# Kernel tuning notes

Measured on AMD Instinct MI355X. Metric: run time of the kernel, lower is better.

The kernel has to match this reference:

```python
import jax, jax.numpy as jnp
import numpy as np

N_NODES = 20000
N_EDGES = 200000
N_FEAT = 2048   # number_of_labels
H1 = 512        # GATE_hidden_size_1
H2 = 30         # GATE_hidden_size_2


def setup_inputs() -> dict:
    key = jax.random.key(0)
    ks = jax.random.split(key, 6)
    s = 0.05
    features = jax.random.normal(ks[0], (N_NODES, N_FEAT), dtype=jnp.float32)
    edge_index = jax.random.randint(ks[1], (2, N_EDGES), 0, N_NODES)
    W1 = jax.random.normal(ks[2], (N_FEAT, H1), dtype=jnp.float32) * s
    att_src1 = jax.random.normal(ks[3], (H1,), dtype=jnp.float32) * s
    att_dst1 = jax.random.normal(ks[4], (H1,), dtype=jnp.float32) * s
    W2 = jax.random.normal(ks[5], (H1, H2), dtype=jnp.float32) * s
    return {"features": features, "edge_index": edge_index,
            "W1": W1, "att_src1": att_src1, "att_dst1": att_dst1, "W2": W2}


def _segment_softmax(e, seg, n):
    # softmax over edges grouped by destination node (every node has a self loop)
    m = jax.ops.segment_max(e, seg, num_segments=n)
    ex = jnp.exp(e - m[seg])
    den = jax.ops.segment_sum(ex, seg, num_segments=n)
    return ex / den[seg]


def _gat_propagate(xw, a_src, a_dst, src, dst, n):
    # STAGATE GATConv message: alpha = sigmoid(a_src[j] + a_dst[i]), segment-softmax, scatter-add
    e = jax.nn.sigmoid(a_src[src] + a_dst[dst])          # [E]
    coef = _segment_softmax(e, dst, n)                   # [E]
    msg = xw[src] * coef[:, None]                        # [E, C] gather + scale
    return jax.ops.segment_sum(msg, dst, num_segments=n)  # [N, C] scatter-add


def reference(features, edge_index, W1, att_src1, att_dst1, W2):
    n = features.shape[0]
    loops = jnp.arange(n, dtype=edge_index.dtype)
    src = jnp.concatenate([edge_index[0], loops])  # add_self_loops=True
    dst = jnp.concatenate([edge_index[1], loops])

    # conv1 (attention=True): computes and stores node-level attention logits
    xw1 = features @ W1                 # [N, H1]
    a1s = xw1 @ att_src1                # [N]
    a1d = xw1 @ att_dst1                # [N]
    h1 = jax.nn.elu(_gat_propagate(xw1, a1s, a1d, src, dst, n))

    # conv2 (attention=False): plain linear transform, no propagation
    h2 = h1 @ W2                        # [N, H2]
    norm = jnp.sqrt(jnp.sum(h2 * h2, axis=1, keepdims=True))
    h2 = h2 / jnp.maximum(norm, 1e-12)  # F.normalize(dim=1)

    # conv3: weight tied to W2^T, attention tied to conv1's logits
    xw3 = h2 @ W2.T                     # [N, H1]
    h3 = jax.nn.elu(_gat_propagate(xw3, a1s, a1d, src, dst, n))

    # conv4 (attention=False): weight tied to W1^T
    h4 = h3 @ W1.T                      # [N, N_FEAT]

    return jnp.mean((features - h4) ** 2)  # F.mse_loss
```

## Files before the change

kernel.cpp:

```cpp
#include <hip/hip_runtime.h>
#include <math.h>

#define N_NODES 20000
#define N_EDGESI 200000
#define E_TOT   220000
#define N_FEAT  2048
#define H1      512
#define H2      30

typedef __bf16 bf16x8 __attribute__((ext_vector_type(8)));
typedef float  floatx4 __attribute__((ext_vector_type(4)));

__device__ __forceinline__ unsigned short f2bf(float f) {
    unsigned int u = __float_as_uint(f);
    unsigned int r = (u + 0x7FFF + ((u >> 16) & 1)) >> 16;
    return (unsigned short)r;
}
__device__ __forceinline__ float bf2f(unsigned short u) {
    return __uint_as_float(((unsigned int)u) << 16);
}
__device__ __forceinline__ unsigned int packtrunc(float a, float b) {
    return (__float_as_uint(a) >> 16) | (__float_as_uint(b) & 0xFFFF0000u);
}
__device__ __forceinline__ unsigned int packrne(float a, float b) {
    return (unsigned int)f2bf(a) | ((unsigned int)f2bf(b) << 16);
}

__global__ __launch_bounds__(256) void cvtW1(const float* __restrict__ W1,
                                             unsigned short* __restrict__ w1bf,
                                             unsigned short* __restrict__ w1tbf) {
    __shared__ float tile[32][33];
    const int bk = blockIdx.y * 32, bn = blockIdx.x * 32;
    const int tc = threadIdx.x & 31, tr = threadIdx.x >> 5;
    for (int r = tr; r < 32; r += 8) {
        float v = W1[(size_t)(bk + r) * H1 + bn + tc];
        w1bf[(size_t)(bk + r) * H1 + bn + tc] = f2bf(v);
        tile[r][tc] = v;
    }
    __syncthreads();
    for (int r = tr; r < 32; r += 8) {
        w1tbf[(size_t)(bn + r) * N_FEAT + bk + tc] = f2bf(tile[tc][r]);
    }
}

__global__ __launch_bounds__(256, 5) void gemm1_mfma(const float* __restrict__ A,
                                                     const unsigned short* __restrict__ Bt,
                                                     unsigned short* __restrict__ C,
                                                     const float* __restrict__ atts,
                                                     const float* __restrict__ attd,
                                                     float* __restrict__ a1s,
                                                     float* __restrict__ a1d) {
    __shared__ unsigned short As[2][64 * 40];
    __shared__ unsigned short Bs[2][128 * 40];
    const int blk = blockIdx.x;
    const int xcd = blk & 7, rr = blk >> 3;
    const int ntile = rr & 3, group = rr >> 2;
    const int stripe = group * 8 + xcd;
    if (stripe >= 313) return;
    const int bm = stripe * 64, bn = ntile * 128;
    const int t = threadIdx.x;
    const int lane = t & 63, w = t >> 6;
    const int wm = w >> 1, wn = w & 1;
    const int ln = lane & 15, qd = lane >> 4;
    const int r0 = t >> 2, cs = (t & 3) * 8;

    int gra = bm + r0;        if (gra > N_NODES - 1) gra = N_NODES - 1;
    const float* ap0 = A + (size_t)gra * N_FEAT + cs;
    const unsigned short* bp0 = Bt + (size_t)(bn + r0) * N_FEAT + cs;
    const unsigned short* bp1 = Bt + (size_t)(bn + r0 + 64) * N_FEAT + cs;

    floatx4 acc[2][4];
#pragma unroll
    for (int i = 0; i < 2; i++)
#pragma unroll
        for (int j = 0; j < 4; j++) acc[i][j] = (floatx4){0.f, 0.f, 0.f, 0.f};

    float4 pa00 = *(const float4*)(ap0);
    float4 pa01 = *(const float4*)(ap0 + 4);
    uint4  pb0  = *(const uint4*)(bp0);
    uint4  pb1  = *(const uint4*)(bp1);
    {
        uint4 pk0;
        pk0.x = packtrunc(pa00.x, pa00.y); pk0.y = packtrunc(pa00.z, pa00.w);
        pk0.z = packtrunc(pa01.x, pa01.y); pk0.w = packtrunc(pa01.z, pa01.w);
        *(uint4*)&As[0][r0 * 40 + cs] = pk0;
        *(uint4*)&Bs[0][r0 * 40 + cs] = pb0;
        *(uint4*)&Bs[0][(r0 + 64) * 40 + cs] = pb1;
    }
    pa00 = *(const float4*)(ap0 + 32);
    pa01 = *(const float4*)(ap0 + 36);
    pb0  = *(const uint4*)(bp0 + 32);
    pb1  = *(const uint4*)(bp1 + 32);
    __syncthreads();

    int cur = 0;
    for (int k0 = 0; k0 < N_FEAT; k0 += 32) {
        bf16x8 af[2], bfr[4];
        const unsigned short* Ab = &As[cur][(wm * 32 + ln) * 40 + qd * 8];
        const unsigned short* Bb = &Bs[cur][(wn * 64 + ln) * 40 + qd * 8];
#pragma unroll
        for (int i = 0; i < 2; i++) af[i]  = *(const bf16x8*)(const void*)(Ab + i * 16 * 40);
#pragma unroll
        for (int j = 0; j < 4; j++) bfr[j] = *(const bf16x8*)(const void*)(Bb + j * 16 * 40);
        if (k0 + 32 < N_FEAT) {
            uint4 pk0;
            pk0.x = packtrunc(pa00.x, pa00.y); pk0.y = packtrunc(pa00.z, pa00.w);
            pk0.z = packtrunc(pa01.x, pa01.y); pk0.w = packtrunc(pa01.z, pa01.w);
            const int nb = cur ^ 1;
            *(uint4*)&As[nb][r0 * 40 + cs] = pk0;
            *(uint4*)&Bs[nb][r0 * 40 + cs] = pb0;
            *(uint4*)&Bs[nb][(r0 + 64) * 40 + cs] = pb1;
            if (k0 + 64 < N_FEAT) {
                const int kn = k0 + 64;
                pa00 = *(const float4*)(ap0 + kn);
                pa01 = *(const float4*)(ap0 + kn + 4);
                pb0  = *(const uint4*)(bp0 + kn);
                pb1  = *(const uint4*)(bp1 + kn);
            }
        }
#pragma unroll
        for (int i = 0; i < 2; i++)
#pragma unroll
            for (int j = 0; j < 4; j++)
                acc[i][j] = __builtin_amdgcn_mfma_f32_16x16x32_bf16(af[i], bfr[j], acc[i][j], 0, 0, 0);
        if (k0 + 32 < N_FEAT) __syncthreads();
        cur ^= 1;
    }

#pragma unroll
    for (int i = 0; i < 2; i++)
#pragma unroll
        for (int j = 0; j < 4; j++)
#pragma unroll
            for (int p = 0; p < 4; p++) {
                int m = bm + wm * 32 + i * 16 + qd * 4 + p;
                if (m < N_NODES) {
                    int n = bn + wn * 64 + j * 16 + ln;
                    C[(size_t)m * H1 + n] = f2bf(acc[i][j][p]);
                }
            }
    float avs[4], avd[4];
#pragma unroll
    for (int j = 0; j < 4; j++) {
        int n = bn + wn * 64 + j * 16 + ln;
        avs[j] = atts[n];
        avd[j] = attd[n];
    }
#pragma unroll
    for (int i = 0; i < 2; i++)
#pragma unroll
        for (int p = 0; p < 4; p++) {
            float vs = 0.f, vd = 0.f;
#pragma unroll
            for (int j = 0; j < 4; j++) {
                vs += acc[i][j][p] * avs[j];
                vd += acc[i][j][p] * avd[j];
            }
#pragma unroll
            for (int msk = 1; msk < 16; msk <<= 1) {
                vs += __shfl_xor(vs, msk);
                vd += __shfl_xor(vd, msk);
            }
            if (ln == p) {
                int m = bm + wm * 32 + i * 16 + qd * 4 + p;
                if (m < N_NODES) {
                    unsafeAtomicAdd(a1s + m, vs);
                    unsafeAtomicAdd(a1d + m, vd);
                }
            }
        }
}

__global__ __launch_bounds__(256) void gemm4_mse(const unsigned short* __restrict__ A,
                                                 const unsigned short* __restrict__ B,
                                                 const float* __restrict__ F,
                                                 float* __restrict__ partial) {
    __shared__ unsigned short As[128 * 40];
    __shared__ unsigned short Bs[128 * 40];
    __shared__ float red[256];
    const int blk = blockIdx.x;
    const int xcd = blk & 7, rr = blk >> 3;
    const int ntile = rr & 15, group = rr >> 4;
    const int stripe = group * 8 + xcd;
    if (stripe >= 157) return;
    const int bm = stripe * 128, bn = ntile * 128;
    const int t = threadIdx.x;
    const int lane = t & 63, w = t >> 6;
    const int wm = w >> 1, wn = w & 1;
    const int ln = lane & 15, qd = lane >> 4;
    const int r0 = t >> 2, cs = (t & 3) * 8;

    int gr0 = bm + r0;        if (gr0 > N_NODES - 1) gr0 = N_NODES - 1;
    int gr1 = bm + r0 + 64;   if (gr1 > N_NODES - 1) gr1 = N_NODES - 1;
    const unsigned short* ap0 = A + (size_t)gr0 * H1 + cs;
    const unsigned short* ap1 = A + (size_t)gr1 * H1 + cs;
    const unsigned short* bp0 = B + (size_t)(bn + r0) * H1 + cs;
    const unsigned short* bp1 = B + (size_t)(bn + r0 + 64) * H1 + cs;

    floatx4 acc[4][4];
#pragma unroll
    for (int i = 0; i < 4; i++)
#pragma unroll
        for (int j = 0; j < 4; j++) acc[i][j] = (floatx4){0.f, 0.f, 0.f, 0.f};

    uint4 pa0 = *(const uint4*)(ap0);
    uint4 pa1 = *(const uint4*)(ap1);
    uint4 pb0 = *(const uint4*)(bp0);
    uint4 pb1 = *(const uint4*)(bp1);

    for (int k0 = 0; k0 < H1; k0 += 32) {
        *(uint4*)&As[r0 * 40 + cs] = pa0;
        *(uint4*)&As[(r0 + 64) * 40 + cs] = pa1;
        *(uint4*)&Bs[r0 * 40 + cs] = pb0;
        *(uint4*)&Bs[(r0 + 64) * 40 + cs] = pb1;
        __syncthreads();
        const bool more = (k0 + 32) < H1;
        if (more) {
            int kn = k0 + 32;
            pa0 = *(const uint4*)(ap0 + kn);
            pa1 = *(const uint4*)(ap1 + kn);
            pb0 = *(const uint4*)(bp0 + kn);
            pb1 = *(const uint4*)(bp1 + kn);
        }
        bf16x8 af[4], bfr[4];
        const unsigned short* Ab = As + (size_t)(wm * 64 + ln) * 40 + qd * 8;
        const unsigned short* Bb = Bs + (size_t)(wn * 64 + ln) * 40 + qd * 8;
#pragma unroll
        for (int i = 0; i < 4; i++) af[i]  = *(const bf16x8*)(const void*)(Ab + i * 16 * 40);
#pragma unroll
        for (int j = 0; j < 4; j++) bfr[j] = *(const bf16x8*)(const void*)(Bb + j * 16 * 40);
#pragma unroll
        for (int i = 0; i < 4; i++)
#pragma unroll
            for (int j = 0; j < 4; j++)
                acc[i][j] = __builtin_amdgcn_mfma_f32_16x16x32_bf16(af[i], bfr[j], acc[i][j], 0, 0, 0);
        __syncthreads();
    }
    float sum = 0.f;
#pragma unroll
    for (int i = 0; i < 4; i++)
#pragma unroll
        for (int j = 0; j < 4; j++)
#pragma unroll
            for (int p = 0; p < 4; p++) {
                int m = bm + wm * 64 + i * 16 + qd * 4 + p;
                if (m < N_NODES) {
                    int n = bn + wn * 64 + j * 16 + ln;
                    float fv = F[(size_t)m * N_FEAT + n];
                    float d = fv - acc[i][j][p];
                    sum += d * d;
                }
            }
    red[t] = sum;
    __syncthreads();
    for (int off = 128; off; off >>= 1) {
        if (t < off) red[t] += red[t + off];
        __syncthreads();
    }
    if (t == 0) unsafeAtomicAdd(partial, red[0]);
}

__global__ void edge_att(const int* __restrict__ ei,
                         const float* __restrict__ a1s,
                         const float* __restrict__ a1d,
                         float* __restrict__ ebuf,
                         float* __restrict__ den,
                         int* __restrict__ deg) {
    int e = blockIdx.x * blockDim.x + threadIdx.x;
    if (e >= E_TOT) return;
    int s, d;
    if (e < N_EDGESI) { s = ei[e]; d = ei[N_EDGESI + e]; }
    else { s = e - N_EDGESI; d = s; }
    float x = a1s[s] + a1d[d];
    float sig = 1.f / (1.f + __expf(-x));
    float ex = __expf(sig);
    ebuf[e] = ex;
    unsafeAtomicAdd(&den[d], ex);
    atomicAdd(&deg[d], 1);
}

__global__ __launch_bounds__(1024) void scan_k(const int* __restrict__ deg,
                                               int* __restrict__ off) {
    __shared__ int wsum[16];
    __shared__ int carry_s;
    const int lane = threadIdx.x & 63, wid = threadIdx.x >> 6;
    if (threadIdx.x == 0) carry_s = 0;
    __syncthreads();
    for (int base = 0; base < N_NODES; base += 1024) {
        int i = base + threadIdx.x;
        int v = (i < N_NODES) ? deg[i] : 0;
        int x = v;
#pragma unroll
        for (int s = 1; s < 64; s <<= 1) {
            int tt = __shfl_up(x, s);
            if (lane >= s) x += tt;
        }
        if (lane == 63) wsum[wid] = x;
        __syncthreads();
        if (wid == 0 && lane < 16) {
            int wv = wsum[lane];
#pragma unroll
            for (int s = 1; s < 16; s <<= 1) {
                int tt = __shfl_up(wv, s);
                if (lane >= s) wv += tt;
            }
            wsum[lane] = wv;
        }
        __syncthreads();
        int wbase = (wid == 0) ? 0 : wsum[wid - 1];
        int c = carry_s;
        int incl = x + wbase + c;
        if (i < N_NODES) off[i] = incl - v;
        __syncthreads();
        if (threadIdx.x == 0) carry_s = c + wsum[15];
        __syncthreads();
    }
}

__global__ void bucket_k(const int* __restrict__ ei,
                         const float* __restrict__ ebuf,
                         const float* __restrict__ den,
                         int* __restrict__ cursor,
                         int* __restrict__ csr_src,
                         float* __restrict__ csr_coef) {
    int e = blockIdx.x * blockDim.x + threadIdx.x;
    if (e >= E_TOT) return;
    int s, d;
    if (e < N_EDGESI) { s = ei[e]; d = ei[N_EDGESI + e]; }
    else { s = e - N_EDGESI; d = s; }
    int pos = atomicAdd(&cursor[d], 1);
    csr_src[pos] = s;
    csr_coef[pos] = ebuf[e] / den[d];
}

__global__ __launch_bounds__(256) void gather_elu_bf(const int* __restrict__ off,
                                                     const int* __restrict__ csr_src,
                                                     const float* __restrict__ csr_coef,
                                                     const unsigned short* __restrict__ X,
                                                     unsigned short* __restrict__ Y) {
    int d = blockIdx.x * 4 + (threadIdx.x >> 6);
    int lane = threadIdx.x & 63;
    if (d >= N_NODES) return;
    int beg = off[d];
    int end = (d == N_NODES - 1) ? E_TOT : off[d + 1];
    float a[8] = {0.f, 0.f, 0.f, 0.f, 0.f, 0.f, 0.f, 0.f};
    float b[8] = {0.f, 0.f, 0.f, 0.f, 0.f, 0.f, 0.f, 0.f};
    int j = beg;
    for (; j + 1 < end; j += 2) {
        int s0 = csr_src[j], s1 = csr_src[j + 1];
        float c0 = csr_coef[j], c1 = csr_coef[j + 1];
        uint4 raw0 = *(const uint4*)(X + (size_t)s0 * H1 + lane * 8);
        uint4 raw1 = *(const uint4*)(X + (size_t)s1 * H1 + lane * 8);
        a[0] += __uint_as_float(raw0.x << 16) * c0;
        a[1] += __uint_as_float(raw0.x & 0xFFFF0000u) * c0;
        a[2] += __uint_as_float(raw0.y << 16) * c0;
        a[3] += __uint_as_float(raw0.y & 0xFFFF0000u) * c0;
        a[4] += __uint_as_float(raw0.z << 16) * c0;
        a[5] += __uint_as_float(raw0.z & 0xFFFF0000u) * c0;
        a[6] += __uint_as_float(raw0.w << 16) * c0;
        a[7] += __uint_as_float(raw0.w & 0xFFFF0000u) * c0;
        b[0] += __uint_as_float(raw1.x << 16) * c1;
        b[1] += __uint_as_float(raw1.x & 0xFFFF0000u) * c1;
        b[2] += __uint_as_float(raw1.y << 16) * c1;
        b[3] += __uint_as_float(raw1.y & 0xFFFF0000u) * c1;
        b[4] += __uint_as_float(raw1.z << 16) * c1;
        b[5] += __uint_as_float(raw1.z & 0xFFFF0000u) * c1;
        b[6] += __uint_as_float(raw1.w << 16) * c1;
        b[7] += __uint_as_float(raw1.w & 0xFFFF0000u) * c1;
    }
    if (j < end) {
        int s0 = csr_src[j];
        float c0 = csr_coef[j];
        uint4 raw0 = *(const uint4*)(X + (size_t)s0 * H1 + lane * 8);
        a[0] += __uint_as_float(raw0.x << 16) * c0;
        a[1] += __uint_as_float(raw0.x & 0xFFFF0000u) * c0;
        a[2] += __uint_as_float(raw0.y << 16) * c0;
        a[3] += __uint_as_float(raw0.y & 0xFFFF0000u) * c0;
        a[4] += __uint_as_float(raw0.z << 16) * c0;
        a[5] += __uint_as_float(raw0.z & 0xFFFF0000u) * c0;
        a[6] += __uint_as_float(raw0.w << 16) * c0;
        a[7] += __uint_as_float(raw0.w & 0xFFFF0000u) * c0;
    }
#pragma unroll
    for (int e = 0; e < 8; e++) {
        float v = a[e] + b[e];
        a[e] = v > 0.f ? v : __expf(v) - 1.f;
    }
    uint4 o;
    o.x = packrne(a[0], a[1]);
    o.y = packrne(a[2], a[3]);
    o.z = packrne(a[4], a[5]);
    o.w = packrne(a[6], a[7]);
    *(uint4*)(Y + (size_t)d * H1 + lane * 8) = o;
}

__global__ __launch_bounds__(256) void gemm2_norm_bf(const unsigned short* __restrict__ H1b,
                                                     const float* __restrict__ W2,
                                                     float* __restrict__ h2n) {
    __shared__ float hs[8 * 516];
    const int n0 = blockIdx.x * 8;
    const int tid = threadIdx.x;
    for (int idx = tid; idx < 512; idx += 256) {
        int r = idx >> 6, c = (idx & 63) * 8;
        uint4 raw = *(const uint4*)(H1b + (size_t)(n0 + r) * H1 + c);
        float* hp = hs + r * 516 + c;
        hp[0] = __uint_as_float(raw.x << 16);
        hp[1] = __uint_as_float(raw.x & 0xFFFF0000u);
        hp[2] = __uint_as_float(raw.y << 16);
        hp[3] = __uint_as_float(raw.y & 0xFFFF0000u);
        hp[4] = __uint_as_float(raw.z << 16);
        hp[5] = __uint_as_float(raw.z & 0xFFFF0000u);
        hp[6] = __uint_as_float(raw.w << 16);
        hp[7] = __uint_as_float(raw.w & 0xFFFF0000u);
    }
    __syncthreads();
    const int sub = tid >> 5, j = tid & 31;
    float a0 = 0.f, a1 = 0.f, a2 = 0.f, a3 = 0.f;
    if (j < H2) {
        const float* hr = hs + sub * 516;
        for (int k = 0; k < H1; k += 4) {
            a0 += hr[k] * W2[k * H2 + j];
            a1 += hr[k + 1] * W2[(k + 1) * H2 + j];
            a2 += hr[k + 2] * W2[(k + 2) * H2 + j];
            a3 += hr[k + 3] * W2[(k + 3) * H2 + j];
        }
    }
    float acc = (a0 + a1) + (a2 + a3);
    float sq = acc * acc;
    for (int m = 16; m; m >>= 1) sq += __shfl_xor(sq, m, 32);
    float inv = 1.f / fmaxf(sqrtf(sq), 1e-12f);
    if (j < H2) h2n[(size_t)(n0 + sub) * H2 + j] = acc * inv;
}

#define G3_CHUNK 40
__global__ __launch_bounds__(256) void gemm3_k(const float* __restrict__ h2n,
                                               const float* __restrict__ W2,
                                               unsigned short* __restrict__ xw3) {
    const int t = threadIdx.x;
    const int h0 = t << 1;
    float w0[H2], w1[H2];
#pragma unroll
    for (int k = 0; k < H2; k++) {
        w0[k] = W2[(size_t)h0 * H2 + k];
        w1[k] = W2[(size_t)h0 * H2 + H2 + k];
    }
    const int n0 = blockIdx.x * G3_CHUNK;
    const int nend = (n0 + G3_CHUNK < N_NODES) ? n0 + G3_CHUNK : N_NODES;
    for (int n = n0; n < nend; n++) {
        const float* hr = h2n + (size_t)n * H2;
        float a0 = 0.f, a1 = 0.f;
#pragma unroll
        for (int k = 0; k < H2; k++) {
            float hv = hr[k];
            a0 += hv * w0[k];
            a1 += hv * w1[k];
        }
        *(unsigned int*)(xw3 + (size_t)n * H1 + h0) = packrne(a0, a1);
    }
}

__global__ void finalize_k(const float* __restrict__ partial, float* __restrict__ out) {
    out[0] = partial[0] * (1.f / ((float)N_NODES * (float)N_FEAT));
}

extern "C" void kernel_launch(void* const* d_in, const int* in_sizes, int n_in,
                              void* d_out, int out_size, void* d_ws, size_t ws_size,
                              hipStream_t stream) {
    const float* features = (const float*)d_in[0];
    const int*   ei       = (const int*)d_in[1];
    const float* W1       = (const float*)d_in[2];
    const float* atts     = (const float*)d_in[3];
    const float* attd     = (const float*)d_in[4];
    const float* W2       = (const float*)d_in[5];
    float* out = (float*)d_out;

    char* ws = (char*)d_ws;
    unsigned short* xw1bf = (unsigned short*)(ws);
    unsigned short* h3bf  = (unsigned short*)(ws + 20480000);
    unsigned short* h1bf  = (unsigned short*)(ws + 40960000);
    unsigned short* w1bf  = (unsigned short*)(ws + 61440000);
    unsigned short* w1tbf = (unsigned short*)(ws + 63537152);
    float* h2n      = (float*)(ws + 65634304);
    float* a1s      = (float*)(ws + 68034304);
    float* a1d      = (float*)(ws + 68114304);
    float* den      = (float*)(ws + 68194304);
    int*   deg      = (int*)  (ws + 68274304);
    float* partial  = (float*)(ws + 68354304);
    float* ebuf     = (float*)(ws + 68354320);
    int*   off      = (int*)  (ws + 69234320);
    int*   cursor   = (int*)  (ws + 69314320);
    int*   csr_src  = (int*)  (ws + 69394320);
    float* csr_coef = (float*)(ws + 70274320);

    hipMemsetAsync(a1s, 0, 320016, stream);

    cvtW1<<<dim3(16, 64), 256, 0, stream>>>(W1, w1bf, w1tbf);

    gemm1_mfma<<<1280, 256, 0, stream>>>(features, w1tbf, xw1bf, atts, attd, a1s, a1d);

    edge_att<<<(E_TOT + 255) / 256, 256, 0, stream>>>(ei, a1s, a1d, ebuf, den, deg);

    scan_k<<<1, 1024, 0, stream>>>(deg, off);
    hipMemcpyAsync(cursor, off, 20000 * 4, hipMemcpyDeviceToDevice, stream);
    bucket_k<<<(E_TOT + 255) / 256, 256, 0, stream>>>(ei, ebuf, den, cursor, csr_src, csr_coef);

    gather_elu_bf<<<N_NODES / 4, 256, 0, stream>>>(off, csr_src, csr_coef, xw1bf, h1bf);

    gemm2_norm_bf<<<N_NODES / 8, 256, 0, stream>>>(h1bf, W2, h2n);

    gemm3_k<<<(N_NODES + G3_CHUNK - 1) / G3_CHUNK, 256, 0, stream>>>(h2n, W2, xw1bf);

    gather_elu_bf<<<N_NODES / 4, 256, 0, stream>>>(off, csr_src, csr_coef, xw1bf, h3bf);

    gemm4_mse<<<2560, 256, 0, stream>>>(h3bf, w1bf, features, partial);

    finalize_k<<<1, 1, 0, stream>>>(partial, out);
}
```

Before: 626.5 us.

## Use direct global-to-LDS loads with triple-buffered swizzled pipeline in GEMMs

Both the first GEMM and the final GEMM+MSE kernel now stage tiles via global_load_lds (direct global-to-LDS DMA) into three rotating XOR-swizzled LDS buffers, with waitcnt-based barriers that keep two stages in flight. In gemm1 the fp32 feature tile is now stored as fp32 in LDS and truncated to bf16 at fragment load time rather than before the LDS store. The aim is to remove register round-trips and hide global latency better, at the cost of more LDS per block (occupancy hints lowered to 3) and doubled LDS traffic for the fp32 A tile.

```diff
diff --git a/kernel.cpp b/kernel.cpp
--- a/kernel.cpp
+++ b/kernel.cpp
@@ -11,19 +11,33 @@
 typedef __bf16 bf16x8 __attribute__((ext_vector_type(8)));
 typedef float  floatx4 __attribute__((ext_vector_type(4)));
 
+__device__ __forceinline__ void gl16(const void* g, void* l) {
+    __builtin_amdgcn_global_load_lds(
+        (const __attribute__((address_space(1))) unsigned int*)g,
+        (__attribute__((address_space(3))) unsigned int*)l, 16, 0, 0);
+}
+__device__ __forceinline__ void stage_barrier4() {
+    asm volatile("s_waitcnt vmcnt(4) lgkmcnt(0)" ::: "memory");
+    __builtin_amdgcn_s_barrier();
+}
+__device__ __forceinline__ void stage_barrier0() {
+    asm volatile("s_waitcnt vmcnt(0) lgkmcnt(0)" ::: "memory");
+    __builtin_amdgcn_s_barrier();
+}
+
 __device__ __forceinline__ unsigned short f2bf(float f) {
     unsigned int u = __float_as_uint(f);
     unsigned int r = (u + 0x7FFF + ((u >> 16) & 1)) >> 16;
     return (unsigned short)r;
 }
-__device__ __forceinline__ float bf2f(unsigned short u) {
-    return __uint_as_float(((unsigned int)u) << 16);
-}
 __device__ __forceinline__ unsigned int packtrunc(float a, float b) {
     return (__float_as_uint(a) >> 16) | (__float_as_uint(b) & 0xFFFF0000u);
 }
 __device__ __forceinline__ unsigned int packrne(float a, float b) {
     return (unsigned int)f2bf(a) | ((unsigned int)f2bf(b) << 16);
+}
+__device__ __forceinline__ bf16x8 u4_to_bf(uint4 u) {
+    union { uint4 u; bf16x8 b; } cv; cv.u = u; return cv.b;
 }
 
 __global__ __launch_bounds__(256) void cvtW1(const float* __restrict__ W1,
@@ -43,15 +57,15 @@
     }
 }
 
-__global__ __launch_bounds__(256, 5) void gemm1_mfma(const float* __restrict__ A,
+__global__ __launch_bounds__(256, 3) void gemm1_mfma(const float* __restrict__ A,
                                                      const unsigned short* __restrict__ Bt,
                                                      unsigned short* __restrict__ C,
                                                      const float* __restrict__ atts,
                                                      const float* __restrict__ attd,
                                                      float* __restrict__ a1s,
                                                      float* __restrict__ a1d) {
-    __shared__ unsigned short As[2][64 * 40];
-    __shared__ unsigned short Bs[2][128 * 40];
+    __shared__ float          Asb[3][64 * 32];
+    __shared__ unsigned short Bsb[3][128 * 32];
     const int blk = blockIdx.x;
     const int xcd = blk & 7, rr = blk >> 3;
     const int ntile = rr & 3, group = rr >> 2;
@@ -62,12 +76,41 @@
     const int lane = t & 63, w = t >> 6;
     const int wm = w >> 1, wn = w & 1;
     const int ln = lane & 15, qd = lane >> 4;
-    const int r0 = t >> 2, cs = (t & 3) * 8;
-
-    int gra = bm + r0;        if (gra > N_NODES - 1) gra = N_NODES - 1;
-    const float* ap0 = A + (size_t)gra * N_FEAT + cs;
-    const unsigned short* bp0 = Bt + (size_t)(bn + r0) * N_FEAT + cs;
-    const unsigned short* bp1 = Bt + (size_t)(bn + r0 + 64) * N_FEAT + cs;
+
+    const int ci0 = t, ci1 = t + 256;
+    const int ar0 = ci0 >> 3, ap0 = ci0 & 7;
+    const int ar1 = ci1 >> 3, ap1 = ci1 & 7;
+    int gra0 = bm + ar0; if (gra0 > N_NODES - 1) gra0 = N_NODES - 1;
+    int gra1 = bm + ar1; if (gra1 > N_NODES - 1) gra1 = N_NODES - 1;
+    const float* gA0 = A + (size_t)gra0 * N_FEAT + ((ap0 ^ (ar0 & 7)) << 2);
+    const float* gA1 = A + (size_t)gra1 * N_FEAT + ((ap1 ^ (ar1 & 7)) << 2);
+    const int ldsA0 = ci0 * 4, ldsA1 = ci1 * 4;
+    const int br0 = ci0 >> 2, bp0 = ci0 & 3;
+    const int br1 = ci1 >> 2, bp1 = ci1 & 3;
+    const unsigned short* gB0 = Bt + (size_t)(bn + br0) * N_FEAT + ((bp0 ^ ((br0 >> 1) & 3)) << 3);
+    const unsigned short* gB1 = Bt + (size_t)(bn + br1) * N_FEAT + ((bp1 ^ ((br1 >> 1) & 3)) << 3);
+    const int ldsB0 = ci0 * 8, ldsB1 = ci1 * 8;
+
+#define STAGE1(k0, Ab, Bb) do { \
+        gl16(gA0 + (k0), (Ab) + ldsA0); \
+        gl16(gA1 + (k0), (Ab) + ldsA1); \
+        gl16(gB0 + (k0), (Bb) + ldsB0); \
+        gl16(gB1 + (k0), (Bb) + ldsB1); \
+    } while (0)
+
+    int offA[2][2], offB[4];
+#pragma unroll
+    for (int i = 0; i < 2; i++) {
+        int row = wm * 32 + i * 16 + ln;
+#pragma unroll
+        for (int h = 0; h < 2; h++)
+            offA[i][h] = row * 32 + (((qd * 2 + h) ^ (row & 7)) << 2);
+    }
+#pragma unroll
+    for (int j = 0; j < 4; j++) {
+        int row = wn * 64 + j * 16 + ln;
+        offB[j] = row * 32 + ((qd ^ ((row >> 1) & 3)) << 3);
+    }
 
     floatx4 acc[2][4];
 #pragma unroll
@@ -75,57 +118,42 @@
 #pragma unroll
         for (int j = 0; j < 4; j++) acc[i][j] = (floatx4){0.f, 0.f, 0.f, 0.f};
 
-    float4 pa00 = *(const float4*)(ap0);
-    float4 pa01 = *(const float4*)(ap0 + 4);
-    uint4  pb0  = *(const uint4*)(bp0);
-    uint4  pb1  = *(const uint4*)(bp1);
-    {
-        uint4 pk0;
-        pk0.x = packtrunc(pa00.x, pa00.y); pk0.y = packtrunc(pa00.z, pa00.w);
-        pk0.z = packtrunc(pa01.x, pa01.y); pk0.w = packtrunc(pa01.z, pa01.w);
-        *(uint4*)&As[0][r0 * 40 + cs] = pk0;
-        *(uint4*)&Bs[0][r0 * 40 + cs] = pb0;
-        *(uint4*)&Bs[0][(r0 + 64) * 40 + cs] = pb1;
-    }
-    pa00 = *(const float4*)(ap0 + 32);
-    pa01 = *(const float4*)(ap0 + 36);
-    pb0  = *(const uint4*)(bp0 + 32);
-    pb1  = *(const uint4*)(bp1 + 32);
-    __syncthreads();
-
-    int cur = 0;
-    for (int k0 = 0; k0 < N_FEAT; k0 += 32) {
-        bf16x8 af[2], bfr[4];
-        const unsigned short* Ab = &As[cur][(wm * 32 + ln) * 40 + qd * 8];
-        const unsigned short* Bb = &Bs[cur][(wn * 64 + ln) * 40 + qd * 8];
-#pragma unroll
-        for (int i = 0; i < 2; i++) af[i]  = *(const bf16x8*)(const void*)(Ab + i * 16 * 40);
-#pragma unroll
-        for (int j = 0; j < 4; j++) bfr[j] = *(const bf16x8*)(const void*)(Bb + j * 16 * 40);
-        if (k0 + 32 < N_FEAT) {
-            uint4 pk0;
-            pk0.x = packtrunc(pa00.x, pa00.y); pk0.y = packtrunc(pa00.z, pa00.w);
-            pk0.z = packtrunc(pa01.x, pa01.y); pk0.w = packtrunc(pa01.z, pa01.w);
-            const int nb = cur ^ 1;
-            *(uint4*)&As[nb][r0 * 40 + cs] = pk0;
-            *(uint4*)&Bs[nb][r0 * 40 + cs] = pb0;
-            *(uint4*)&Bs[nb][(r0 + 64) * 40 + cs] = pb1;
-            if (k0 + 64 < N_FEAT) {
-                const int kn = k0 + 64;
-                pa00 = *(const float4*)(ap0 + kn);
-                pa01 = *(const float4*)(ap0 + kn + 4);
-                pb0  = *(const uint4*)(bp0 + kn);
-                pb1  = *(const uint4*)(bp1 + kn);
-            }
-        }
-#pragma unroll
-        for (int i = 0; i < 2; i++)
-#pragma unroll
-            for (int j = 0; j < 4; j++)
-                acc[i][j] = __builtin_amdgcn_mfma_f32_16x16x32_bf16(af[i], bfr[j], acc[i][j], 0, 0, 0);
-        if (k0 + 32 < N_FEAT) __syncthreads();
-        cur ^= 1;
-    }
+#define COMPUTE1(Ab, Bb) do { \
+        bf16x8 af_[2], bf_[4]; \
+        _Pragma("unroll") for (int j = 0; j < 4; j++) \
+            bf_[j] = *(const bf16x8*)(const void*)((Bb) + offB[j]); \
+        _Pragma("unroll") for (int i = 0; i < 2; i++) { \
+            float4 f0 = *(const float4*)((Ab) + offA[i][0]); \
+            float4 f1 = *(const float4*)((Ab) + offA[i][1]); \
+            uint4 pk; \
+            pk.x = packtrunc(f0.x, f0.y); pk.y = packtrunc(f0.z, f0.w); \
+            pk.z = packtrunc(f1.x, f1.y); pk.w = packtrunc(f1.z, f1.w); \
+            af_[i] = u4_to_bf(pk); } \
+        _Pragma("unroll") for (int i = 0; i < 2; i++) \
+        _Pragma("unroll") for (int j = 0; j < 4; j++) \
+            acc[i][j] = __builtin_amdgcn_mfma_f32_16x16x32_bf16(af_[i], bf_[j], acc[i][j], 0, 0, 0); \
+    } while (0)
+
+    float *Ac = Asb[0], *An1 = Asb[1], *An2 = Asb[2];
+    unsigned short *Bc = Bsb[0], *Bn1 = Bsb[1], *Bn2 = Bsb[2];
+    STAGE1(0, Ac, Bc);
+    STAGE1(32, An1, Bn1);
+    stage_barrier4();
+
+    for (int k = 0; k < 62; ++k) {
+        STAGE1((k + 2) * 32, An2, Bn2);
+        COMPUTE1(Ac, Bc);
+        stage_barrier4();
+        float* ta = Ac; Ac = An1; An1 = An2; An2 = ta;
+        unsigned short* tb = Bc; Bc = Bn1; Bn1 = Bn2; Bn2 = tb;
+    }
+    COMPUTE1(Ac, Bc);
+    stage_barrier0();
+    { float* ta = Ac; Ac = An1; An1 = An2; An2 = ta;
+      unsigned short* tb = Bc; Bc = Bn1; Bn1 = Bn2; Bn2 = tb; }
+    COMPUTE1(Ac, Bc);
+#undef STAGE1
+#undef COMPUTE1
 
 #pragma unroll
     for (int i = 0; i < 2; i++)
@@ -171,12 +199,12 @@
         }
 }
 
-__global__ __launch_bounds__(256) void gemm4_mse(const unsigned short* __restrict__ A,
-                                                 const unsigned short* __restrict__ B,
-                                                 const float* __restrict__ F,
-                                                 float* __restrict__ partial) {
-    __shared__ unsigned short As[128 * 40];
-    __shared__ unsigned short Bs[128 * 40];
+__global__ __launch_bounds__(256, 3) void gemm4_mse(const unsigned short* __restrict__ Ah,
+                                                    const unsigned short* __restrict__ B,
+                                                    const float* __restrict__ F,
+                                                    float* __restrict__ partial) {
+    __shared__ unsigned short Asb[3][128 * 32];
+    __shared__ unsigned short Bsb[3][128 * 32];
     __shared__ float red[256];
     const int blk = blockIdx.x;
     const int xcd = blk & 7, rr = blk >> 3;
@@ -188,14 +216,36 @@
     const int lane = t & 63, w = t >> 6;
     const int wm = w >> 1, wn = w & 1;
     const int ln = lane & 15, qd = lane >> 4;
-    const int r0 = t >> 2, cs = (t & 3) * 8;
-
-    int gr0 = bm + r0;        if (gr0 > N_NODES - 1) gr0 = N_NODES - 1;
-    int gr1 = bm + r0 + 64;   if (gr1 > N_NODES - 1) gr1 = N_NODES - 1;
-    const unsigned short* ap0 = A + (size_t)gr0 * H1 + cs;
-    const unsigned short* ap1 = A + (size_t)gr1 * H1 + cs;
-    const unsigned short* bp0 = B + (size_t)(bn + r0) * H1 + cs;
-    const unsigned short* bp1 = B + (size_t)(bn + r0 + 64) * H1 + cs;
+
+    const int ci0 = t, ci1 = t + 256;
+    const int r0c = ci0 >> 2, p0c = ci0 & 3;
+    const int r1c = ci1 >> 2, p1c = ci1 & 3;
+    int gra0 = bm + r0c; if (gra0 > N_NODES - 1) gra0 = N_NODES - 1;
+    int gra1 = bm + r1c; if (gra1 > N_NODES - 1) gra1 = N_NODES - 1;
+    const unsigned short* gA0 = Ah + (size_t)gra0 * H1 + ((p0c ^ ((r0c >> 1) & 3)) << 3);
+    const unsigned short* gA1 = Ah + (size_t)gra1 * H1 + ((p1c ^ ((r1c >> 1) & 3)) << 3);
+    const unsigned short* gB0 = B + (size_t)(bn + r0c) * H1 + ((p0c ^ ((r0c >> 1) & 3)) << 3);
+    const unsigned short* gB1 = B + (size_t)(bn + r1c) * H1 + ((p1c ^ ((r1c >> 1) & 3)) << 3);
+    const int lds0 = ci0 * 8, lds1 = ci1 * 8;
+
+#define STAGE4(k0, Ab, Bb) do { \
+        gl16(gA0 + (k0), (Ab) + lds0); \
+        gl16(gA1 + (k0), (Ab) + lds1); \
+        gl16(gB0 + (k0), (Bb) + lds0); \
+        gl16(gB1 + (k0), (Bb) + lds1); \
+    } while (0)
+
+    int offA[4], offB[4];
+#pragma unroll
+    for (int i = 0; i < 4; i++) {
+        int row = wm * 64 + i * 16 + ln;
+        offA[i] = row * 32 + ((qd ^ ((row >> 1) & 3)) << 3);
+    }
+#pragma unroll
+    for (int j = 0; j < 4; j++) {
+        int row = wn * 64 + j * 16 + ln;
+        offB[j] = row * 32 + ((qd ^ ((row >> 1) & 3)) << 3);
+    }
 
     floatx4 acc[4][4];
 #pragma unroll
@@ -203,39 +253,38 @@
 #pragma unroll
         for (int j = 0; j < 4; j++) acc[i][j] = (floatx4){0.f, 0.f, 0.f, 0.f};
 
-    uint4 pa0 = *(const uint4*)(ap0);
-    uint4 pa1 = *(const uint4*)(ap1);
-    uint4 pb0 = *(const uint4*)(bp0);
-    uint4 pb1 = *(const uint4*)(bp1);
-
-    for (int k0 = 0; k0 < H1; k0 += 32) {
-        *(uint4*)&As[r0 * 40 + cs] = pa0;
-        *(uint4*)&As[(r0 + 64) * 40 + cs] = pa1;
-        *(uint4*)&Bs[r0 * 40 + cs] = pb0;
-        *(uint4*)&Bs[(r0 + 64) * 40 + cs] = pb1;
-        __syncthreads();
-        const bool more = (k0 + 32) < H1;
-        if (more) {
-            int kn = k0 + 32;
-            pa0 = *(const uint4*)(ap0 + kn);
-            pa1 = *(const uint4*)(ap1 + kn);
-            pb0 = *(const uint4*)(bp0 + kn);
-            pb1 = *(const uint4*)(bp1 + kn);
-        }
-        bf16x8 af[4], bfr[4];
-        const unsigned short* Ab = As + (size_t)(wm * 64 + ln) * 40 + qd * 8;
-        const unsigned short* Bb = Bs + (size_t)(wn * 64 + ln) * 40 + qd * 8;
-#pragma unroll
-        for (int i = 0; i < 4; i++) af[i]  = *(const bf16x8*)(const void*)(Ab + i * 16 * 40);
-#pragma unroll
-        for (int j = 0; j < 4; j++) bfr[j] = *(const bf16x8*)(const void*)(Bb + j * 16 * 40);
-#pragma unroll
-        for (int i = 0; i < 4; i++)
-#pragma unroll
-            for (int j = 0; j < 4; j++)
-                acc[i][j] = __builtin_amdgcn_mfma_f32_16x16x32_bf16(af[i], bfr[j], acc[i][j], 0, 0, 0);
-        __syncthreads();
-    }
+#define COMPUTE4(Ab, Bb) do { \
+        bf16x8 af_[4], bf_[4]; \
+        _Pragma("unroll") for (int i = 0; i < 4; i++) \
+            af_[i] = *(const bf16x8*)(const void*)((Ab) + offA[i]); \
+        _Pragma("unroll") for (int j = 0; j < 4; j++) \
+            bf_[j] = *(const bf16x8*)(const void*)((Bb) + offB[j]); \
+        _Pragma("unroll") for (int i = 0; i < 4; i++) \
+        _Pragma("unroll") for (int j = 0; j < 4; j++) \
+            acc[i][j] = __builtin_amdgcn_mfma_f32_16x16x32_bf16(af_[i], bf_[j], acc[i][j], 0, 0, 0); \
+    } while (0)
+
+    unsigned short *Ac = Asb[0], *An1 = Asb[1], *An2 = Asb[2];
+    unsigned short *Bc = Bsb[0], *Bn1 = Bsb[1], *Bn2 = Bsb[2];
+    STAGE4(0, Ac, Bc);
+    STAGE4(32, An1, Bn1);
+    stage_barrier4();
+
+    for (int k = 0; k < 14; ++k) {
+        STAGE4((k + 2) * 32, An2, Bn2);
+        COMPUTE4(Ac, Bc);
+        stage_barrier4();
+        unsigned short* ta = Ac; Ac = An1; An1 = An2; An2 = ta;
+        unsigned short* tb = Bc; Bc = Bn1; Bn1 = Bn2; Bn2 = tb;
+    }
+    COMPUTE4(Ac, Bc);
+    stage_barrier0();
+    { unsigned short* ta = Ac; Ac = An1; An1 = An2; An2 = ta;
+      unsigned short* tb = Bc; Bc = Bn1; Bn1 = Bn2; Bn2 = tb; }
+    COMPUTE4(Ac, Bc);
+#undef STAGE4
+#undef COMPUTE4
+
     float sum = 0.f;
 #pragma unroll
     for (int i = 0; i < 4; i++)
```

Result: slower. 651.5 us (+4.0%).

## Load B fragments directly to registers in GEMMs, shrink gemm4 tile

Applied to the files above, without the earlier changes.

Both MFMA GEMMs (gemm1 and gemm4) now skip staging the B operand through LDS. Each lane loads its B fragment straight from global memory into registers, double-buffered two k-steps ahead. Only A is staged in a double-buffered LDS tile, and the barrier becomes a manual lgkmcnt wait plus s_barrier. gemm4 moves to 64-row tiles with twice the blocks and a 5-wave occupancy hint, which cuts LDS traffic and barrier cost. In exchange, B reads are less coalesced per lane (16 rows × 16 bytes each), register pressure rises, and gemm4 reads B twice as often overall.

```diff
diff --git a/kernel.cpp b/kernel.cpp
--- a/kernel.cpp
+++ b/kernel.cpp
@@ -11,19 +11,24 @@
 typedef __bf16 bf16x8 __attribute__((ext_vector_type(8)));
 typedef float  floatx4 __attribute__((ext_vector_type(4)));
 
+__device__ __forceinline__ void lds_barrier() {
+    asm volatile("s_waitcnt lgkmcnt(0)" ::: "memory");
+    __builtin_amdgcn_s_barrier();
+}
+
 __device__ __forceinline__ unsigned short f2bf(float f) {
     unsigned int u = __float_as_uint(f);
     unsigned int r = (u + 0x7FFF + ((u >> 16) & 1)) >> 16;
     return (unsigned short)r;
 }
-__device__ __forceinline__ float bf2f(unsigned short u) {
-    return __uint_as_float(((unsigned int)u) << 16);
-}
 __device__ __forceinline__ unsigned int packtrunc(float a, float b) {
     return (__float_as_uint(a) >> 16) | (__float_as_uint(b) & 0xFFFF0000u);
 }
 __device__ __forceinline__ unsigned int packrne(float a, float b) {
     return (unsigned int)f2bf(a) | ((unsigned int)f2bf(b) << 16);
+}
+__device__ __forceinline__ bf16x8 u4_to_bf(uint4 u) {
+    union { uint4 u; bf16x8 b; } cv; cv.u = u; return cv.b;
 }
 
 __global__ __launch_bounds__(256) void cvtW1(const float* __restrict__ W1,
@@ -51,7 +56,6 @@
                                                      float* __restrict__ a1s,
                                                      float* __restrict__ a1d) {
     __shared__ unsigned short As[2][64 * 40];
-    __shared__ unsigned short Bs[2][128 * 40];
     const int blk = blockIdx.x;
     const int xcd = blk & 7, rr = blk >> 3;
     const int ntile = rr & 3, group = rr >> 2;
@@ -64,10 +68,16 @@
     const int ln = lane & 15, qd = lane >> 4;
     const int r0 = t >> 2, cs = (t & 3) * 8;
 
-    int gra = bm + r0;        if (gra > N_NODES - 1) gra = N_NODES - 1;
-    const float* ap0 = A + (size_t)gra * N_FEAT + cs;
-    const unsigned short* bp0 = Bt + (size_t)(bn + r0) * N_FEAT + cs;
-    const unsigned short* bp1 = Bt + (size_t)(bn + r0 + 64) * N_FEAT + cs;
+    int gra = bm + r0; if (gra > N_NODES - 1) gra = N_NODES - 1;
+    const float* apA = A + (size_t)gra * N_FEAT + cs;
+
+    const unsigned short* bfp[4];
+#pragma unroll
+    for (int j = 0; j < 4; j++)
+        bfp[j] = Bt + (size_t)(bn + wn * 64 + j * 16 + ln) * N_FEAT + qd * 8;
+
+    const int offA0 = (wm * 32 + ln) * 40 + qd * 8;
+    const int offA1 = (wm * 32 + 16 + ln) * 40 + qd * 8;
 
     floatx4 acc[2][4];
 #pragma unroll
@@ -75,57 +85,58 @@
 #pragma unroll
         for (int j = 0; j < 4; j++) acc[i][j] = (floatx4){0.f, 0.f, 0.f, 0.f};
 
-    float4 pa00 = *(const float4*)(ap0);
-    float4 pa01 = *(const float4*)(ap0 + 4);
-    uint4  pb0  = *(const uint4*)(bp0);
-    uint4  pb1  = *(const uint4*)(bp1);
     {
-        uint4 pk0;
-        pk0.x = packtrunc(pa00.x, pa00.y); pk0.y = packtrunc(pa00.z, pa00.w);
-        pk0.z = packtrunc(pa01.x, pa01.y); pk0.w = packtrunc(pa01.z, pa01.w);
-        *(uint4*)&As[0][r0 * 40 + cs] = pk0;
-        *(uint4*)&Bs[0][r0 * 40 + cs] = pb0;
-        *(uint4*)&Bs[0][(r0 + 64) * 40 + cs] = pb1;
-    }
-    pa00 = *(const float4*)(ap0 + 32);
-    pa01 = *(const float4*)(ap0 + 36);
-    pb0  = *(const uint4*)(bp0 + 32);
-    pb1  = *(const uint4*)(bp1 + 32);
-    __syncthreads();
-
-    int cur = 0;
-    for (int k0 = 0; k0 < N_FEAT; k0 += 32) {
-        bf16x8 af[2], bfr[4];
-        const unsigned short* Ab = &As[cur][(wm * 32 + ln) * 40 + qd * 8];
-        const unsigned short* Bb = &Bs[cur][(wn * 64 + ln) * 40 + qd * 8];
-#pragma unroll
-        for (int i = 0; i < 2; i++) af[i]  = *(const bf16x8*)(const void*)(Ab + i * 16 * 40);
-#pragma unroll
-        for (int j = 0; j < 4; j++) bfr[j] = *(const bf16x8*)(const void*)(Bb + j * 16 * 40);
-        if (k0 + 32 < N_FEAT) {
-            uint4 pk0;
-            pk0.x = packtrunc(pa00.x, pa00.y); pk0.y = packtrunc(pa00.z, pa00.w);
-            pk0.z = packtrunc(pa01.x, pa01.y); pk0.w = packtrunc(pa01.z, pa01.w);
-            const int nb = cur ^ 1;
-            *(uint4*)&As[nb][r0 * 40 + cs] = pk0;
-            *(uint4*)&Bs[nb][r0 * 40 + cs] = pb0;
-            *(uint4*)&Bs[nb][(r0 + 64) * 40 + cs] = pb1;
-            if (k0 + 64 < N_FEAT) {
-                const int kn = k0 + 64;
-                pa00 = *(const float4*)(ap0 + kn);
-                pa01 = *(const float4*)(ap0 + kn + 4);
-                pb0  = *(const uint4*)(bp0 + kn);
-                pb1  = *(const uint4*)(bp1 + kn);
-            }
-        }
-#pragma unroll
-        for (int i = 0; i < 2; i++)
-#pragma unroll
-            for (int j = 0; j < 4; j++)
-                acc[i][j] = __builtin_amdgcn_mfma_f32_16x16x32_bf16(af[i], bfr[j], acc[i][j], 0, 0, 0);
-        if (k0 + 32 < N_FEAT) __syncthreads();
-        cur ^= 1;
-    }
+        float4 a0 = *(const float4*)(apA);
+        float4 a1 = *(const float4*)(apA + 4);
+        uint4 pk;
+        pk.x = packtrunc(a0.x, a0.y); pk.y = packtrunc(a0.z, a0.w);
+        pk.z = packtrunc(a1.x, a1.y); pk.w = packtrunc(a1.z, a1.w);
+        *(uint4*)&As[0][r0 * 40 + cs] = pk;
+    }
+    float4 pa0 = *(const float4*)(apA + 32);
+    float4 pa1 = *(const float4*)(apA + 36);
+    uint4 b0[4], b1[4];
+#pragma unroll
+    for (int j = 0; j < 4; j++) b0[j] = *(const uint4*)(bfp[j]);
+#pragma unroll
+    for (int j = 0; j < 4; j++) b1[j] = *(const uint4*)(bfp[j] + 32);
+    lds_barrier();
+
+#define G1_ITER(BUF, BR, kk) do { \
+        bf16x8 af0 = *(const bf16x8*)(const void*)&As[BUF][offA0]; \
+        bf16x8 af1 = *(const bf16x8*)(const void*)&As[BUF][offA1]; \
+        if ((kk) + 1 < 64) { \
+            uint4 pk; \
+            pk.x = packtrunc(pa0.x, pa0.y); pk.y = packtrunc(pa0.z, pa0.w); \
+            pk.z = packtrunc(pa1.x, pa1.y); pk.w = packtrunc(pa1.z, pa1.w); \
+            *(uint4*)&As[(BUF) ^ 1][r0 * 40 + cs] = pk; \
+        } \
+        if ((kk) + 2 < 64) { \
+            pa0 = *(const float4*)(apA + ((kk) + 2) * 32); \
+            pa1 = *(const float4*)(apA + ((kk) + 2) * 32 + 4); \
+        } \
+        bf16x8 bfr0 = u4_to_bf(BR[0]), bfr1 = u4_to_bf(BR[1]); \
+        bf16x8 bfr2 = u4_to_bf(BR[2]), bfr3 = u4_to_bf(BR[3]); \
+        if ((kk) + 2 < 64) { \
+            _Pragma("unroll") for (int j = 0; j < 4; j++) \
+                BR[j] = *(const uint4*)(bfp[j] + ((kk) + 2) * 32); \
+        } \
+        acc[0][0] = __builtin_amdgcn_mfma_f32_16x16x32_bf16(af0, bfr0, acc[0][0], 0, 0, 0); \
+        acc[0][1] = __builtin_amdgcn_mfma_f32_16x16x32_bf16(af0, bfr1, acc[0][1], 0, 0, 0); \
+        acc[0][2] = __builtin_amdgcn_mfma_f32_16x16x32_bf16(af0, bfr2, acc[0][2], 0, 0, 0); \
+        acc[0][3] = __builtin_amdgcn_mfma_f32_16x16x32_bf16(af0, bfr3, acc[0][3], 0, 0, 0); \
+        acc[1][0] = __builtin_amdgcn_mfma_f32_16x16x32_bf16(af1, bfr0, acc[1][0], 0, 0, 0); \
+        acc[1][1] = __builtin_amdgcn_mfma_f32_16x16x32_bf16(af1, bfr1, acc[1][1], 0, 0, 0); \
+        acc[1][2] = __builtin_amdgcn_mfma_f32_16x16x32_bf16(af1, bfr2, acc[1][2], 0, 0, 0); \
+        acc[1][3] = __builtin_amdgcn_mfma_f32_16x16x32_bf16(af1, bfr3, acc[1][3], 0, 0, 0); \
+        if ((kk) + 1 < 64) lds_barrier(); \
+    } while (0)
+
+    for (int k = 0; k < 64; k += 2) {
+        G1_ITER(0, b0, k);
+        G1_ITER(1, b1, k + 1);
+    }
+#undef G1_ITER
 
 #pragma unroll
     for (int i = 0; i < 2; i++)
@@ -171,79 +182,93 @@
         }
 }
 
-__global__ __launch_bounds__(256) void gemm4_mse(const unsigned short* __restrict__ A,
-                                                 const unsigned short* __restrict__ B,
-                                                 const float* __restrict__ F,
-                                                 float* __restrict__ partial) {
-    __shared__ unsigned short As[128 * 40];
-    __shared__ unsigned short Bs[128 * 40];
+__global__ __launch_bounds__(256, 5) void gemm4_mse(const unsigned short* __restrict__ Ah,
+                                                    const unsigned short* __restrict__ B,
+                                                    const float* __restrict__ F,
+                                                    float* __restrict__ partial) {
+    __shared__ unsigned short As[2][64 * 40];
     __shared__ float red[256];
     const int blk = blockIdx.x;
     const int xcd = blk & 7, rr = blk >> 3;
     const int ntile = rr & 15, group = rr >> 4;
     const int stripe = group * 8 + xcd;
-    if (stripe >= 157) return;
-    const int bm = stripe * 128, bn = ntile * 128;
+    if (stripe >= 313) return;
+    const int bm = stripe * 64, bn = ntile * 128;
     const int t = threadIdx.x;
     const int lane = t & 63, w = t >> 6;
     const int wm = w >> 1, wn = w & 1;
     const int ln = lane & 15, qd = lane >> 4;
     const int r0 = t >> 2, cs = (t & 3) * 8;
 
-    int gr0 = bm + r0;        if (gr0 > N_NODES - 1) gr0 = N_NODES - 1;
-    int gr1 = bm + r0 + 64;   if (gr1 > N_NODES - 1) gr1 = N_NODES - 1;
-    const unsigned short* ap0 = A + (size_t)gr0 * H1 + cs;
-    const unsigned short* ap1 = A + (size_t)gr1 * H1 + cs;
-    const unsigned short* bp0 = B + (size_t)(bn + r0) * H1 + cs;
-    const unsigned short* bp1 = B + (size_t)(bn + r0 + 64) * H1 + cs;
-
-    floatx4 acc[4][4];
-#pragma unroll
-    for (int i = 0; i < 4; i++)
+    int gra = bm + r0; if (gra > N_NODES - 1) gra = N_NODES - 1;
+    const unsigned short* apA = Ah + (size_t)gra * H1 + cs;
+
+    const unsigned short* bfp[4];
+#pragma unroll
+    for (int j = 0; j < 4; j++)
+        bfp[j] = B + (size_t)(bn + wn * 64 + j * 16 + ln) * H1 + qd * 8;
+
+    const int offA0 = (wm * 32 + ln) * 40 + qd * 8;
+    const int offA1 = (wm * 32 + 16 + ln) * 40 + qd * 8;
+
+    floatx4 acc[2][4];
+#pragma unroll
+    for (int i = 0; i < 2; i++)
 #pragma unroll
         for (int j = 0; j < 4; j++) acc[i][j] = (floatx4){0.f, 0.f, 0.f, 0.f};
 
-    uint4 pa0 = *(const uint4*)(ap0);
-    uint4 pa1 = *(const uint4*)(ap1);
-    uint4 pb0 = *(const uint4*)(bp0);
-    uint4 pb1 = *(const uint4*)(bp1);
-
-    for (int k0 = 0; k0 < H1; k0 += 32) {
-        *(uint4*)&As[r0 * 40 + cs] = pa0;
-        *(uint4*)&As[(r0 + 64) * 40 + cs] = pa1;
-        *(uint4*)&Bs[r0 * 40 + cs] = pb0;
-        *(uint4*)&Bs[(r0 + 64) * 40 + cs] = pb1;
-        __syncthreads();
-        const bool more = (k0 + 32) < H1;
-        if (more) {
-            int kn = k0 + 32;
-            pa0 = *(const uint4*)(ap0 + kn);
-            pa1 = *(const uint4*)(ap1 + kn);
-            pb0 = *(const uint4*)(bp0 + kn);
-            pb1 = *(const uint4*)(bp1 + kn);
-        }
-        bf16x8 af[4], bfr[4];
-        const unsigned short* Ab = As + (size_t)(wm * 64 + ln) * 40 + qd * 8;
-        const unsigned short* Bb = Bs + (size_t)(wn * 64 + ln) * 40 + qd * 8;
-#pragma unroll
-        for (int i = 0; i < 4; i++) af[i]  = *(const bf16x8*)(const void*)(Ab + i * 16 * 40);
-#pragma unroll
-        for (int j = 0; j < 4; j++) bfr[j] = *(const bf16x8*)(const void*)(Bb + j * 16 * 40);
-#pragma unroll
-        for (int i = 0; i < 4; i++)
-#pragma unroll
-            for (int j = 0; j < 4; j++)
-                acc[i][j] = __builtin_amdgcn_mfma_f32_16x16x32_bf16(af[i], bfr[j], acc[i][j], 0, 0, 0);
-        __syncthreads();
-    }
+    {
+        uint4 pk = *(const uint4*)(apA);
+        *(uint4*)&As[0][r0 * 40 + cs] = pk;
+    }
+    uint4 pa = *(const uint4*)(apA + 32);
+    uint4 b0[4], b1[4];
+#pragma unroll
+    for (int j = 0; j < 4; j++) b0[j] = *(const uint4*)(bfp[j]);
+#pragma unroll
+    for (int j = 0; j < 4; j++) b1[j] = *(const uint4*)(bfp[j] + 32);
+    lds_barrier();
+
+#define G4_ITER(BUF, BR, kk) do { \
+        bf16x8 af0 = *(const bf16x8*)(const void*)&As[BUF][offA0]; \
+        bf16x8 af1 = *(const bf16x8*)(const void*)&As[BUF][offA1]; \
+        if ((kk) + 1 < 16) { \
+            *(uint4*)&As[(BUF) ^ 1][r0 * 40 + cs] = pa; \
+        } \
+        if ((kk) + 2 < 16) { \
+            pa = *(const uint4*)(apA + ((kk) + 2) * 32); \
+        } \
+        bf16x8 bfr0 = u4_to_bf(BR[0]), bfr1 = u4_to_bf(BR[1]); \
+        bf16x8 bfr2 = u4_to_bf(BR[2]), bfr3 = u4_to_bf(BR[3]); \
+        if ((kk) + 2 < 16) { \
+            _Pragma("unroll") for (int j = 0; j < 4; j++) \
+                BR[j] = *(const uint4*)(bfp[j] + ((kk) + 2) * 32); \
+        } \
+        acc[0][0] = __builtin_amdgcn_mfma_f32_16x16x32_bf16(af0, bfr0, acc[0][0], 0, 0, 0); \
+        acc[0][1] = __builtin_amdgcn_mfma_f32_16x16x32_bf16(af0, bfr1, acc[0][1], 0, 0, 0); \
+        acc[0][2] = __builtin_amdgcn_mfma_f32_16x16x32_bf16(af0, bfr2, acc[0][2], 0, 0, 0); \
+        acc[0][3] = __builtin_amdgcn_mfma_f32_16x16x32_bf16(af0, bfr3, acc[0][3], 0, 0, 0); \
+        acc[1][0] = __builtin_amdgcn_mfma_f32_16x16x32_bf16(af1, bfr0, acc[1][0], 0, 0, 0); \
+        acc[1][1] = __builtin_amdgcn_mfma_f32_16x16x32_bf16(af1, bfr1, acc[1][1], 0, 0, 0); \
+        acc[1][2] = __builtin_amdgcn_mfma_f32_16x16x32_bf16(af1, bfr2, acc[1][2], 0, 0, 0); \
+        acc[1][3] = __builtin_amdgcn_mfma_f32_16x16x32_bf16(af1, bfr3, acc[1][3], 0, 0, 0); \
+        if ((kk) + 1 < 16) lds_barrier(); \
+    } while (0)
+
+    for (int k = 0; k < 16; k += 2) {
+        G4_ITER(0, b0, k);
+        G4_ITER(1, b1, k + 1);
+    }
+#undef G4_ITER
+
     float sum = 0.f;
 #pragma unroll
-    for (int i = 0; i < 4; i++)
+    for (int i = 0; i < 2; i++)
 #pragma unroll
         for (int j = 0; j < 4; j++)
 #pragma unroll
             for (int p = 0; p < 4; p++) {
-                int m = bm + wm * 64 + i * 16 + qd * 4 + p;
+                int m = bm + wm * 32 + i * 16 + qd * 4 + p;
                 if (m < N_NODES) {
                     int n = bn + wn * 64 + j * 16 + ln;
                     float fv = F[(size_t)m * N_FEAT + n];
@@ -512,7 +537,7 @@
 
     gather_elu_bf<<<N_NODES / 4, 256, 0, stream>>>(off, csr_src, csr_coef, xw1bf, h3bf);
 
-    gemm4_mse<<<2560, 256, 0, stream>>>(h3bf, w1bf, features, partial);
+    gemm4_mse<<<5120, 256, 0, stream>>>(h3bf, w1bf, features, partial);
 
     finalize_k<<<1, 1, 0, stream>>>(partial, out);
 }
```

Measured after the change: 976.6 us. +55.9%, slower.
